# Kernel optimization log

Measured on AMD Instinct MI355X. Metric: run time of the kernel, lower is better.

The kernel has to match this reference:

```python
import jax, jax.numpy as jnp
import numpy as np

B, L, DIM, ET, NH, SD, NC = 32, 200, 36, 128, 64, 9, 2


def setup_inputs() -> dict:
    key = jax.random.key(0)
    ks = jax.random.split(key, 16)
    f = jnp.float32
    vals = jax.random.normal(ks[0], (B, L, DIM), f)
    obs = (jax.random.uniform(ks[1], (B, L, DIM)) < 0.7).astype(f)  # 0/1 observation mask
    x = jnp.concatenate([vals, obs], -1)                            # (B, L, 2*DIM)
    time_steps = jnp.sort(jax.random.uniform(ks[2], (B, L)), axis=1)
    static_info = jax.random.normal(ks[3], (B, SD), f)
    query_param = jnp.linspace(0.0, 1.0, ET, dtype=f)               # nn.Parameter(linspace)

    def lin(k, o, i, s):
        return jax.random.normal(k, (o, i), f) * s

    return dict(
        x=x, time_steps=time_steps, static_info=static_info, query_param=query_param,
        periodic_w=lin(ks[4], ET - 1, 1, 1.0), periodic_b=jnp.zeros((ET - 1,), f),
        timelin_w=lin(ks[5], 1, 1, 1.0), timelin_b=jnp.zeros((1,), f),
        qw=lin(ks[6], ET, ET, ET ** -0.5), qb=jnp.zeros((ET,), f),
        kw=lin(ks[7], ET, ET, ET ** -0.5), kb=jnp.zeros((ET,), f),
        ow=lin(ks[8], DIM, 2 * DIM, (2 * DIM) ** -0.5), ob=jnp.zeros((DIM,), f),
        gru_w_ih=lin(ks[9], 3 * NH, DIM, DIM ** -0.5),
        gru_w_hh=lin(ks[10], 3 * NH, NH, NH ** -0.5),
        gru_b_ih=jnp.zeros((3 * NH,), f), gru_b_hh=jnp.zeros((3 * NH,), f),
        st_w=lin(ks[11], 8, SD, SD ** -0.5), st_b=jnp.zeros((8,), f),
        c1_w=lin(ks[12], NH + 8, NH + 8, (NH + 8) ** -0.5), c1_b=jnp.zeros((NH + 8,), f),
        bn_g=jnp.ones((NH + 8,), f), bn_b=jnp.zeros((NH + 8,), f),
        c2_w=lin(ks[13], NC, NH + 8, (NH + 8) ** -0.5), c2_b=jnp.zeros((NC,), f),
        rand_mask=jax.random.randint(ks[14], (B, L), 0, 2, jnp.int32),
    )


def reference(x, time_steps, static_info, query_param, periodic_w, periodic_b,
              timelin_w, timelin_b, qw, qb, kw, kb, ow, ob,
              gru_w_ih, gru_w_hh, gru_b_ih, gru_b_hh, st_w, st_b,
              c1_w, c1_b, bn_g, bn_b, c2_w, c2_b, rand_mask):
    dim = x.shape[-1] // 2
    irr = x[:, :, dim:]                                   # observation mask channels
    temp = rand_mask.astype(x.dtype)[:, :, None]          # random_masking keep-mask
    m_small = irr * temp
    irr2 = jnp.concatenate([irr, irr], -1)                # (B, L, 2*dim)
    m2 = jnp.concatenate([m_small, m_small], -1)

    def time_emb(tt):
        tt = tt[..., None]
        return jnp.concatenate([tt @ timelin_w.T + timelin_b,
                                jnp.sin(tt @ periodic_w.T + periodic_b)], -1)

    key_e = time_emb(time_steps)                          # (B, L, ET)
    query_e = time_emb(query_param[None, :])[0]           # (ET, ET)
    q = query_e @ qw.T + qb                               # num_heads=1 => dk=ET
    k = key_e @ kw.T + kb
    scores = jnp.einsum('qd,bld->bql', q, k) / jnp.sqrt(jnp.asarray(ET, x.dtype))

    def mta(mask):
        # per-channel masked softmax over keys l: (B, Lq, L, 2*dim)
        s5 = jnp.where(mask[:, None, :, :] == 0, jnp.asarray(-1e9, x.dtype),
                       scores[:, :, :, None])
        p = jax.nn.softmax(s5, axis=2)
        o = jnp.einsum('bqld,bld->bqd', p, x)             # (B, Lq, 2*dim)
        return o @ ow.T + ob                              # (B, Lq, dim)

    out_te = mta(irr2)
    out1_te = mta(m2)

    sx = x[:, :, :dim]
    sx_g = jnp.round(jax.nn.sigmoid(jnp.einsum('bld,ble->bde', sx, sx)))
    sout = jax.nn.sigmoid(jnp.einsum('bqd,bqe->bde', out_te, out_te))

    def step(h, xt):  # torch GRU cell, gate order r,z,n
        gi = xt @ gru_w_ih.T + gru_b_ih
        gh = h @ gru_w_hh.T + gru_b_hh
        ir, iz, inn = jnp.split(gi, 3, -1)
        hr, hz, hn = jnp.split(gh, 3, -1)
        r = jax.nn.sigmoid(ir + hr)
        z = jax.nn.sigmoid(iz + hz)
        n = jnp.tanh(inn + r * hn)
        return (1 - z) * n + z * h, None

    h0 = jnp.zeros((x.shape[0], gru_w_hh.shape[1]), x.dtype)
    h_fin, _ = jax.lax.scan(step, h0, jnp.swapaxes(out_te, 0, 1))

    st = static_info @ st_w.T + st_b
    cls_in = jnp.concatenate([h_fin, st], 1)
    z1 = cls_in @ c1_w.T + c1_b
    mu = z1.mean(0)
    var = z1.var(0)                                       # BatchNorm1d (training stats)
    zn = (z1 - mu) / jnp.sqrt(var + 1e-5) * bn_g + bn_b
    zg = jax.nn.gelu(zn, approximate=False)
    logits = zg @ c2_w.T + c2_b
    return (out_te, out1_te, logits, sx_g, sout, query_param)
```

## Files before the change

### kernel.cpp

```cpp
#include <hip/hip_runtime.h>

#define B_   32
#define L_   200
#define DIM_ 36
#define ET_  128
#define NH_  64
#define SD_  9
#define NC_  2

#define O_TE   0
#define O_T1   147456
#define O_LG   294912
#define O_SXG  294976
#define O_SOUT 336448
#define O_QP   377920

typedef __fp16 half_t;
typedef __attribute__((ext_vector_type(2))) __fp16 half2_t;

__device__ __forceinline__ float sigm(float x) { return 1.f / (1.f + expf(-x)); }
__device__ __forceinline__ float fsigm(float x) {
  return __builtin_amdgcn_rcpf(1.f + __expf(-x));
}
__device__ __forceinline__ float ftanh(float x) {
  return 2.f * __builtin_amdgcn_rcpf(1.f + __expf(-2.f * x)) - 1.f;
}
__device__ __forceinline__ half2_t f2h2(float a, float b) {
  return __builtin_amdgcn_cvt_pkrtz(a, b);
}
__device__ __forceinline__ float dot2acc(half2_t w, half2_t h, float acc) {
#if __has_builtin(__builtin_amdgcn_fdot2)
  return __builtin_amdgcn_fdot2(w, h, acc, false);
#else
  return acc + (float)w.x * (float)h.x + (float)w.y * (float)h.y;
#endif
}

__global__ __launch_bounds__(256) void k_pre2(
    const float* __restrict__ qw, const float* __restrict__ kw,
    const float* __restrict__ qb, const float* __restrict__ qp,
    const float* __restrict__ pw, const float* __restrict__ pb,
    const float* __restrict__ tlw, const float* __restrict__ tlb,
    const float* __restrict__ x, float* __restrict__ qm2,
    float* __restrict__ xmean, float* __restrict__ out) {
  int blk = blockIdx.x, t = threadIdx.x;
  if (blk < 128) {
    __shared__ float eq[128];
    __shared__ float uq[128];
    int q = blk;
    if (t < 128) {
      float tt = qp[q];
      eq[t] = (t == 0) ? tt * tlw[0] + tlb[0]
                       : __sinf(tt * pw[t - 1] + pb[t - 1]);
    }
    __syncthreads();
    if (t < 128) {
      const float4* qw4 = (const float4*)(qw + (size_t)t * 128);
      float a = qb[t];
      #pragma unroll 8
      for (int c = 0; c < 32; c++) {
        float4 w = qw4[c];
        a += eq[4 * c] * w.x + eq[4 * c + 1] * w.y +
             eq[4 * c + 2] * w.z + eq[4 * c + 3] * w.w;
      }
      uq[t] = a;
    }
    __syncthreads();
    if (t < 128) {
      float a = 0.f;
      #pragma unroll 8
      for (int i = 0; i < 128; i++) a += uq[i] * kw[i * 128 + t];
      qm2[q * 128 + t] = a * 0.088388347648318447f;
      if (q == 0) out[O_QP + t] = qp[t];
    }
    return;
  }
  int b = blk - 128;
  __shared__ __align__(16) float sxs[L_][76];
  const float4* xsrc = (const float4*)(x + (size_t)b * L_ * 72);
  for (int idx = t; idx < L_ * 18; idx += 256) {
    int l = idx / 18, c = idx % 18;
    ((float4*)&sxs[l][0])[c] = xsrc[l * 18 + c];
  }
  __syncthreads();
  if (t < 72) {
    float s = 0.f;
    #pragma unroll 8
    for (int l = 0; l < L_; l++) s += sxs[l][t];
    xmean[b * 72 + t] = s * (1.0f / L_);
  }
  for (int idx = t; idx < DIM_ * DIM_; idx += 256) {
    int d = idx / DIM_, e = idx % DIM_;
    float s = 0.f;
    #pragma unroll 8
    for (int l = 0; l < L_; l++) s += sxs[l][d] * sxs[l][e];
    out[O_SXG + (size_t)b * DIM_ * DIM_ + idx] = rintf(sigm(s));
  }
}

__global__ __launch_bounds__(1024, 1) void k_attn(
    const float* __restrict__ qm, const float* __restrict__ ts,
    const float* __restrict__ pw, const float* __restrict__ pb,
    const float* __restrict__ tlw, const float* __restrict__ tlb,
    const float* __restrict__ x, const int* __restrict__ rm,
    const float* __restrict__ xmean, const float* __restrict__ ow,
    const float* __restrict__ ob, const float* __restrict__ wih,
    const float* __restrict__ bih, const float* __restrict__ bhh,
    float* __restrict__ gis, float* __restrict__ out) {
  __shared__ __align__(16) char Abuf[103936];
  __shared__ __align__(16) float qs[16][128];
  __shared__ __align__(16) float sc[16][200];
  __shared__ __align__(16) float owsh[DIM_][72];
  float*   ksA  = (float*)Abuf;
  half2_t* wsh2 = (half2_t*)Abuf;
  float*   wihs = (float*)Abuf;
  float*   ote_t = (float*)(Abuf + 28416);
  float*   sums = (float*)(Abuf + 57600);
  float*   ofr  = (float*)(Abuf + 57600 + 36864);

  int b = blockIdx.x >> 3;
  int q0 = (blockIdx.x & 7) << 4;
  int tid = threadIdx.x;

  const float4* qsrc = (const float4*)(qm + q0 * ET_);
  for (int i = tid; i < 16 * 32; i += 1024) ((float4*)qs)[i] = qsrc[i];
  const float4* owsrc = (const float4*)ow;
  for (int i = tid; i < DIM_ * 18; i += 1024) ((float4*)owsh)[i] = owsrc[i];
  {
    float tl_w = tlw[0], tl_b = tlb[0];
    const float* tsb = ts + b * L_;
    for (int i = tid; i < L_ * 128; i += 1024) {
      int l = i >> 7, j = i & 127;
      float t = tsb[l];
      float e = (j == 0) ? t * tl_w + tl_b : __sinf(t * pw[j - 1] + pb[j - 1]);
      int blkj = (j >> 2) ^ ((l >> 2) & 7);
      ksA[(l << 7) + (blkj << 2) + (j & 3)] = e;
    }
  }
  __syncthreads();

  {
    int w = tid >> 6, lg = tid & 63;
    int qp2 = w >> 1;
    int lh = w & 1;
    float acc[2][2];
    #pragma unroll
    for (int i = 0; i < 2; i++)
      #pragma unroll
      for (int j = 0; j < 2; j++) acc[i][j] = 0.f;
    const float4* ks4 = (const float4*)ksA;
    const float4* qs4 = (const float4*)qs;
    int lbase = 100 * lh + 2 * lg;
    int swz0 = (lbase >> 2) & 7;
    int swz1 = ((lbase + 1) >> 2) & 7;
    #pragma unroll 4
    for (int d4 = 0; d4 < 32; d4++) {
      float4 kv[2];
      {
        int l0c = (lbase < 100 * lh + 100) ? lbase : (100 * lh + 99);
        int l1c = (lbase + 1 < 100 * lh + 100) ? lbase + 1 : (100 * lh + 99);
        kv[0] = ks4[(l0c << 5) + (d4 ^ swz0)];
        kv[1] = ks4[(l1c << 5) + (d4 ^ swz1)];
      }
      #pragma unroll
      for (int i = 0; i < 2; i++) {
        float4 qv = qs4[(2 * qp2 + i) * 32 + d4];
        #pragma unroll
        for (int j = 0; j < 2; j++)
          acc[i][j] += qv.x * kv[j].x + qv.y * kv[j].y +
                       qv.z * kv[j].z + qv.w * kv[j].w;
      }
    }
    if (2 * lg < 100) {
      #pragma unroll
      for (int i = 0; i < 2; i++) {
        float2 v = {acc[i][0], acc[i][1]};
        *((float2*)(&sc[2 * qp2 + i][lbase])) = v;
      }
    }
  }
  __syncthreads();

  {
    int qi = tid >> 6, li = tid & 63;
    float m = -1e30f;
    for (int l = li; l < L_; l += 64) m = fmaxf(m, sc[qi][l]);
    #pragma unroll
    for (int off = 32; off >= 1; off >>= 1) m = fmaxf(m, __shfl_xor(m, off));
    for (int l = li; l < L_; l += 64) sc[qi][l] = __expf(sc[qi][l] - m);
  }

  {
    const float2* xb2 = (const float2*)(x + (size_t)b * L_ * 72);
    const int* rmb = rm + b * L_;
    for (int i = tid; i < L_ * 72; i += 1024) {
      int l = i / 72, c2 = i % 72;
      int seg = c2 / 18, fh = c2 % 18;
      float2 v = xb2[l * 36 + fh];
      float2 o = xb2[l * 36 + 18 + fh];
      float rr = (float)rmb[l];
      float w0, w1;
      if (seg == 0)      { w0 = o.x * v.x;      w1 = o.y * v.y; }
      else if (seg == 1) { w0 = o.x;            w1 = o.y; }
      else if (seg == 2) { w0 = o.x * v.x * rr; w1 = o.y * v.y * rr; }
      else               { w0 = o.x * rr;       w1 = o.y * rr; }
      wsh2[l * 72 + c2] = f2h2(w0, w1);
    }
  }
  __syncthreads();

  {
    int quarter = tid >> 8, tt = tid & 255;
    int qi = tt >> 4, li = tt & 15;
    int l0 = quarter * 50;
    float accA[8], accB[8];
    #pragma unroll
    for (int k = 0; k < 8; k++) { accA[k] = 0.f; accB[k] = 0.f; }
    const float4* wA = (const float4*)wsh2;
    #pragma unroll 2
    for (int l = l0; l < l0 + 50; l++) {
      float ev = sc[qi][l];
      float4 wa = wA[l * 18 + li];
      union { float f; half2_t h; } u0, u1, u2, u3;
      u0.f = wa.x; u1.f = wa.y; u2.f = wa.z; u3.f = wa.w;
      accA[0] += ev * (float)u0.h.x; accA[1] += ev * (float)u0.h.y;
      accA[2] += ev * (float)u1.h.x; accA[3] += ev * (float)u1.h.y;
      accA[4] += ev * (float)u2.h.x; accA[5] += ev * (float)u2.h.y;
      accA[6] += ev * (float)u3.h.x; accA[7] += ev * (float)u3.h.y;
      if (li < 2) {
        float4 wb = wA[l * 18 + 16 + li];
        union { float f; half2_t h; } b0, b1, b2, b3;
        b0.f = wb.x; b1.f = wb.y; b2.f = wb.z; b3.f = wb.w;
        accB[0] += ev * (float)b0.h.x; accB[1] += ev * (float)b0.h.y;
        accB[2] += ev * (float)b1.h.x; accB[3] += ev * (float)b1.h.y;
        accB[4] += ev * (float)b2.h.x; accB[5] += ev * (float)b2.h.y;
        accB[6] += ev * (float)b3.h.x; accB[7] += ev * (float)b3.h.y;
      }
    }
    float* sq = sums + quarter * 2304 + qi * 144;
    float4* sA = (float4*)(sq + 8 * li);
    sA[0] = make_float4(accA[0], accA[1], accA[2], accA[3]);
    sA[1] = make_float4(accA[4], accA[5], accA[6], accA[7]);
    if (li < 2) {
      float4* sB = (float4*)(sq + 128 + 8 * li);
      sB[0] = make_float4(accB[0], accB[1], accB[2], accB[3]);
      sB[1] = make_float4(accB[4], accB[5], accB[6], accB[7]);
    }
  }
  __syncthreads();

  const float* xm = xmean + b * 72;
  for (int idx = tid; idx < 192 * 36; idx += 1024) {
    int r = idx / 36, d = idx % 36;
    wihs[r * 37 + d] = wih[idx];
  }
  for (int idx = tid; idx < 16 * DIM_; idx += 1024) {
    int qq = idx / DIM_, j = idx % DIM_;
    const float* s0 = sums + qq * 144;
    const float* s1 = s0 + 2304;
    const float* s2 = s1 + 2304;
    const float* s3 = s2 + 2304;
    float numA = (s0[j] + s1[j]) + (s2[j] + s3[j]);
    float denA = (s0[36 + j] + s1[36 + j]) + (s2[36 + j] + s3[36 + j]);
    float numB = (s0[72 + j] + s1[72 + j]) + (s2[72 + j] + s3[72 + j]);
    float denB = (s0[108 + j] + s1[108 + j]) + (s2[108 + j] + s3[108 + j]);
    float al, ah, bl, bh;
    if (denA > 0.f) { al = numA / denA; ah = 1.f; }
    else            { al = xm[j];       ah = xm[36 + j]; }
    if (denB > 0.f) { bl = numB / denB; bh = 1.f; }
    else            { bl = xm[j];       bh = xm[36 + j]; }
    float* oq = ofr + qq * 144;
    oq[j] = al;      oq[36 + j] = ah;
    oq[72 + j] = bl; oq[108 + j] = bh;
  }
  __syncthreads();

  for (int idx = tid; idx < 16 * 72; idx += 1024) {
    int qq = idx / 72, t = idx % 72;
    int v = t / DIM_, i2 = t % DIM_;
    const float4* o4 = (const float4*)(ofr + qq * 144 + v * 72);
    const float4* w4 = (const float4*)(owsh[i2]);
    float a = ob[i2];
    #pragma unroll
    for (int d4 = 0; d4 < 18; d4++) {
      float4 ov = o4[d4], wv = w4[d4];
      a += ov.x * wv.x + ov.y * wv.y + ov.z * wv.z + ov.w * wv.w;
    }
    size_t off = ((size_t)b * ET_ + q0 + qq) * DIM_ + i2;
    out[(v == 0 ? O_TE : O_T1) + off] = a;
    if (v == 0) ote_t[qq * 36 + i2] = a;
  }
  __syncthreads();

  for (int idx = tid; idx < 16 * 192; idx += 1024) {
    int qq = idx / 192, tt = idx % 192;
    const float* wr = wihs + tt * 37;
    const float* orow = ote_t + qq * 36;
    float a = bih[tt] + ((tt < 2 * NH_) ? bhh[tt] : 0.f);
    #pragma unroll 6
    for (int d = 0; d < 36; d++) a += orow[d] * wr[d];
    gis[((size_t)b * ET_ + q0 + qq) * 192 + tt] = a;
  }
}

__global__ __launch_bounds__(256, 1) void k_sg(
    const float* __restrict__ out_ro, const float* __restrict__ gis,
    const float* __restrict__ whh, const float* __restrict__ bhh,
    float* __restrict__ hfin, float* __restrict__ out) {
  __shared__ __align__(16) float ote_s[ET_][DIM_];
  __shared__ __align__(16) half2_t hpk[NH_ / 2];
  int blk = blockIdx.x, t = threadIdx.x;

  if (blk < 32) {
    int b = blk;
    const float4* osrc = (const float4*)(out_ro + O_TE + (size_t)b * ET_ * DIM_);
    for (int idx = t; idx < ET_ * 9; idx += 256)
      ((float4*)&ote_s[0][0])[idx] = osrc[idx];
    __syncthreads();
    for (int idx = t; idx < DIM_ * DIM_; idx += 256) {
      int d = idx / DIM_, e = idx % DIM_;
      float s = 0.f;
      #pragma unroll 8
      for (int q = 0; q < ET_; q++) s += ote_s[q][d] * ote_s[q][e];
      out[O_SOUT + (size_t)b * DIM_ * DIM_ + idx] = sigm(s);
    }
    return;
  }

  if (t >= 64) return;
  int b = blk - 32;
  const float* gb = gis + (size_t)b * ET_ * 192;

  half2_t wr[32], wz[32], wn[32];
  {
    const float2* r0 = (const float2*)(whh + (size_t)t * NH_);
    const float2* r1 = (const float2*)(whh + (size_t)(NH_ + t) * NH_);
    const float2* r2 = (const float2*)(whh + (size_t)(2 * NH_ + t) * NH_);
    #pragma unroll
    for (int c = 0; c < 32; c++) {
      float2 a = r0[c], bb = r1[c], cc = r2[c];
      wr[c] = f2h2(a.x, a.y);
      wz[c] = f2h2(bb.x, bb.y);
      wn[c] = f2h2(cc.x, cc.y);
    }
  }
  float bh_n = bhh[2 * NH_ + t];

  float pr[2], pz[2], pn[2];
  pr[0] = gb[t];       pz[0] = gb[64 + t];       pn[0] = gb[128 + t];
  pr[1] = gb[192 + t]; pz[1] = gb[192 + 64 + t]; pn[1] = gb[192 + 128 + t];

  float h = 0.f;
  ((half_t*)hpk)[t] = (half_t)0.f;
  for (int q = 0; q < ET_; q++) {
    int s = q & 1;
    float gi_r = pr[s], gi_z = pz[s], gi_n = pn[s];
    if (q + 2 < ET_) {
      const float* g2 = gb + (q + 2) * 192;
      pr[s] = g2[t]; pz[s] = g2[64 + t]; pn[s] = g2[128 + t];
    }
    float ar = 0.f, az = 0.f, an = 0.f;
    const float4* hp4 = (const float4*)hpk;
    #pragma unroll
    for (int c4 = 0; c4 < 8; c4++) {
      float4 hv = hp4[c4];
      union { float f; half2_t h; } u0, u1, u2, u3;
      u0.f = hv.x; u1.f = hv.y; u2.f = hv.z; u3.f = hv.w;
      int c = c4 * 4;
      ar = dot2acc(wr[c + 0], u0.h, ar);
      az = dot2acc(wz[c + 0], u0.h, az);
      an = dot2acc(wn[c + 0], u0.h, an);
      ar = dot2acc(wr[c + 1], u1.h, ar);
      az = dot2acc(wz[c + 1], u1.h, az);
      an = dot2acc(wn[c + 1], u1.h, an);
      ar = dot2acc(wr[c + 2], u2.h, ar);
      az = dot2acc(wz[c + 2], u2.h, az);
      an = dot2acc(wn[c + 2], u2.h, an);
      ar = dot2acc(wr[c + 3], u3.h, ar);
      az = dot2acc(wz[c + 3], u3.h, az);
      an = dot2acc(wn[c + 3], u3.h, an);
    }
    float r = fsigm(gi_r + ar);
    float z = fsigm(gi_z + az);
    float n = ftanh(gi_n + r * (an + bh_n));
    h = n + z * (h - n);
    ((half_t*)hpk)[t] = (half_t)h;
  }
  hfin[b * NH_ + t] = h;
}

__global__ __launch_bounds__(256) void k_cls(
    const float* __restrict__ hfin, const float* __restrict__ si,
    const float* __restrict__ stw, const float* __restrict__ stb,
    const float* __restrict__ c1w, const float* __restrict__ c1b,
    const float* __restrict__ bng, const float* __restrict__ bnb,
    const float* __restrict__ c2w, const float* __restrict__ c2b,
    float* __restrict__ out) {
  __shared__ float cin[B_][72];
  __shared__ float z1[B_][72];
  __shared__ float zg[B_][72];
  int t = threadIdx.x;
  for (int idx = t; idx < B_ * 8; idx += 256) {
    int b = idx / 8, j = idx % 8;
    float acc = stb[j];
    #pragma unroll
    for (int d = 0; d < SD_; d++) acc += si[b * SD_ + d] * stw[j * SD_ + d];
    cin[b][NH_ + j] = acc;
  }
  for (int idx = t; idx < B_ * NH_; idx += 256)
    cin[idx / NH_][idx % NH_] = hfin[idx];
  __syncthreads();
  for (int idx = t; idx < B_ * 72; idx += 256) {
    int b = idx / 72, j = idx % 72;
    float acc = c1b[j];
    #pragma unroll 8
    for (int d = 0; d < 72; d++) acc += cin[b][d] * c1w[j * 72 + d];
    z1[b][j] = acc;
  }
  __syncthreads();
  if (t < 72) {
    float mu = 0.f;
    for (int b = 0; b < B_; b++) mu += z1[b][t];
    mu *= (1.f / B_);
    float vv = 0.f;
    for (int b = 0; b < B_; b++) { float d = z1[b][t] - mu; vv += d * d; }
    vv *= (1.f / B_);
    float inv = 1.f / sqrtf(vv + 1e-5f);
    float g = bng[t], bb = bnb[t];
    for (int b = 0; b < B_; b++) {
      float zn = (z1[b][t] - mu) * inv * g + bb;
      zg[b][t] = 0.5f * zn * (1.f + erff(zn * 0.70710678118654752f));
    }
  }
  __syncthreads();
  for (int idx = t; idx < B_ * NC_; idx += 256) {
    int b = idx / NC_, c = idx % NC_;
    float acc = c2b[c];
    #pragma unroll 8
    for (int d = 0; d < 72; d++) acc += zg[b][d] * c2w[c * 72 + d];
    out[O_LG + idx] = acc;
  }
}

extern "C" void kernel_launch(void* const* d_in, const int* in_sizes, int n_in,
                              void* d_out, int out_size, void* d_ws,
                              size_t ws_size, hipStream_t stream) {
  const float* x    = (const float*)d_in[0];
  const float* ts   = (const float*)d_in[1];
  const float* si   = (const float*)d_in[2];
  const float* qp   = (const float*)d_in[3];
  const float* pw   = (const float*)d_in[4];
  const float* pb   = (const float*)d_in[5];
  const float* tlw  = (const float*)d_in[6];
  const float* tlb  = (const float*)d_in[7];
  const float* qw   = (const float*)d_in[8];
  const float* qb   = (const float*)d_in[9];
  const float* kw   = (const float*)d_in[10];
  const float* ow   = (const float*)d_in[12];
  const float* ob   = (const float*)d_in[13];
  const float* wih  = (const float*)d_in[14];
  const float* whh  = (const float*)d_in[15];
  const float* bih  = (const float*)d_in[16];
  const float* bhh  = (const float*)d_in[17];
  const float* stw  = (const float*)d_in[18];
  const float* stb  = (const float*)d_in[19];
  const float* c1w  = (const float*)d_in[20];
  const float* c1b  = (const float*)d_in[21];
  const float* bng  = (const float*)d_in[22];
  const float* bnb  = (const float*)d_in[23];
  const float* c2w  = (const float*)d_in[24];
  const float* c2b  = (const float*)d_in[25];
  const int*   rm   = (const int*)d_in[26];

  float* out = (float*)d_out;

  float* W = (float*)d_ws;
  float* ws_qm2   = W;
  float* ws_xmean = W + 16384;
  float* ws_hfin  = W + 18688;
  float* ws_gis   = W + 20736;

  hipLaunchKernelGGL(k_pre2, dim3(160), dim3(256), 0, stream,
                     qw, kw, qb, qp, pw, pb, tlw, tlb, x, ws_qm2, ws_xmean,
                     out);
  hipLaunchKernelGGL(k_attn, dim3(B_ * 8), dim3(1024), 0, stream,
                     ws_qm2, ts, pw, pb, tlw, tlb, x, rm, ws_xmean, ow, ob,
                     wih, bih, bhh, ws_gis, out);
  hipLaunchKernelGGL(k_sg, dim3(64), dim3(256), 0, stream,
                     out, ws_gis, whh, bhh, ws_hfin, out);
  hipLaunchKernelGGL(k_cls, dim3(1), dim3(256), 0, stream,
                     ws_hfin, si, stw, stb, c1w, c1b, bng, bnb, c2w, c2b,
                     out);
}
```

Measured before the change: 263.4 us.

## Move GRU input projection from attention kernel into the GRU kernel via shared memory

The GRU input-gate projection (out_te @ W_ih^T + biases) is no longer computed at the end of the attention kernel and written to a global workspace. Instead, each GRU block loads its batch's out_te into shared memory and computes all 128x192 gate inputs into a shared array before the recurrence. This removes a global round trip, an extra sync and the W_ih staging from k_attn, and turns the per-step gate loads into shared reads. The cost is that the projection work moves onto only 32 GRU blocks, using 192 threads each, on the serial critical path.

```diff
diff --git a/kernel.cpp b/kernel.cpp
--- a/kernel.cpp
+++ b/kernel.cpp
@@ -104,17 +104,13 @@
     const float* __restrict__ tlw, const float* __restrict__ tlb,
     const float* __restrict__ x, const int* __restrict__ rm,
     const float* __restrict__ xmean, const float* __restrict__ ow,
-    const float* __restrict__ ob, const float* __restrict__ wih,
-    const float* __restrict__ bih, const float* __restrict__ bhh,
-    float* __restrict__ gis, float* __restrict__ out) {
+    const float* __restrict__ ob, float* __restrict__ out) {
   __shared__ __align__(16) char Abuf[103936];
   __shared__ __align__(16) float qs[16][128];
   __shared__ __align__(16) float sc[16][200];
   __shared__ __align__(16) float owsh[DIM_][72];
   float*   ksA  = (float*)Abuf;
   half2_t* wsh2 = (half2_t*)Abuf;
-  float*   wihs = (float*)Abuf;
-  float*   ote_t = (float*)(Abuf + 28416);
   float*   sums = (float*)(Abuf + 57600);
   float*   ofr  = (float*)(Abuf + 57600 + 36864);
 
@@ -250,10 +246,6 @@
   __syncthreads();
 
   const float* xm = xmean + b * 72;
-  for (int idx = tid; idx < 192 * 36; idx += 1024) {
-    int r = idx / 36, d = idx % 36;
-    wihs[r * 37 + d] = wih[idx];
-  }
   for (int idx = tid; idx < 16 * DIM_; idx += 1024) {
     int qq = idx / DIM_, j = idx % DIM_;
     const float* s0 = sums + qq * 144;
@@ -288,26 +280,16 @@
     }
     size_t off = ((size_t)b * ET_ + q0 + qq) * DIM_ + i2;
     out[(v == 0 ? O_TE : O_T1) + off] = a;
-    if (v == 0) ote_t[qq * 36 + i2] = a;
-  }
-  __syncthreads();
-
-  for (int idx = tid; idx < 16 * 192; idx += 1024) {
-    int qq = idx / 192, tt = idx % 192;
-    const float* wr = wihs + tt * 37;
-    const float* orow = ote_t + qq * 36;
-    float a = bih[tt] + ((tt < 2 * NH_) ? bhh[tt] : 0.f);
-    #pragma unroll 6
-    for (int d = 0; d < 36; d++) a += orow[d] * wr[d];
-    gis[((size_t)b * ET_ + q0 + qq) * 192 + tt] = a;
   }
 }
 
 __global__ __launch_bounds__(256, 1) void k_sg(
-    const float* __restrict__ out_ro, const float* __restrict__ gis,
-    const float* __restrict__ whh, const float* __restrict__ bhh,
-    float* __restrict__ hfin, float* __restrict__ out) {
+    const float* __restrict__ out_ro, const float* __restrict__ wih,
+    const float* __restrict__ bih, const float* __restrict__ whh,
+    const float* __restrict__ bhh, float* __restrict__ hfin,
+    float* __restrict__ out) {
   __shared__ __align__(16) float ote_s[ET_][DIM_];
+  __shared__ float gis[ET_][3 * NH_];
   __shared__ __align__(16) half2_t hpk[NH_ / 2];
   int blk = blockIdx.x, t = threadIdx.x;
 
@@ -327,9 +309,33 @@
     return;
   }
 
+  int b = blk - 32;
+  const float* ote = out_ro + O_TE;
+  const float4* osrc = (const float4*)(ote + (size_t)b * ET_ * DIM_);
+  for (int idx = t; idx < ET_ * DIM_ / 4; idx += 256)
+    ((float4*)&ote_s[0][0])[idx] = osrc[idx];
+  __syncthreads();
+
+  if (t < 3 * NH_) {
+    float wv[DIM_];
+    const float* wrow = wih + (size_t)t * DIM_;
+    #pragma unroll
+    for (int d = 0; d < DIM_; d++) wv[d] = wrow[d];
+    float bi = bih[t] + ((t < 2 * NH_) ? bhh[t] : 0.f);
+    for (int q = 0; q < ET_; q++) {
+      const float4* xr = (const float4*)ote_s[q];
+      float a = bi;
+      #pragma unroll
+      for (int c = 0; c < 9; c++) {
+        float4 xv = xr[c];
+        a += xv.x * wv[4 * c] + xv.y * wv[4 * c + 1] +
+             xv.z * wv[4 * c + 2] + xv.w * wv[4 * c + 3];
+      }
+      gis[q][t] = a;
+    }
+  }
+  __syncthreads();
   if (t >= 64) return;
-  int b = blk - 32;
-  const float* gb = gis + (size_t)b * ET_ * 192;
 
   half2_t wr[32], wz[32], wn[32];
   {
@@ -346,19 +352,12 @@
   }
   float bh_n = bhh[2 * NH_ + t];
 
-  float pr[2], pz[2], pn[2];
-  pr[0] = gb[t];       pz[0] = gb[64 + t];       pn[0] = gb[128 + t];
-  pr[1] = gb[192 + t]; pz[1] = gb[192 + 64 + t]; pn[1] = gb[192 + 128 + t];
-
   float h = 0.f;
   ((half_t*)hpk)[t] = (half_t)0.f;
   for (int q = 0; q < ET_; q++) {
-    int s = q & 1;
-    float gi_r = pr[s], gi_z = pz[s], gi_n = pn[s];
-    if (q + 2 < ET_) {
-      const float* g2 = gb + (q + 2) * 192;
-      pr[s] = g2[t]; pz[s] = g2[64 + t]; pn[s] = g2[128 + t];
-    }
+    float gi_r = gis[q][t];
+    float gi_z = gis[q][NH_ + t];
+    float gi_n = gis[q][2 * NH_ + t];
     float ar = 0.f, az = 0.f, an = 0.f;
     const float4* hp4 = (const float4*)hpk;
     #pragma unroll
@@ -478,16 +477,15 @@
   float* ws_qm2   = W;
   float* ws_xmean = W + 16384;
   float* ws_hfin  = W + 18688;
-  float* ws_gis   = W + 20736;
 
   hipLaunchKernelGGL(k_pre2, dim3(160), dim3(256), 0, stream,
                      qw, kw, qb, qp, pw, pb, tlw, tlb, x, ws_qm2, ws_xmean,
                      out);
   hipLaunchKernelGGL(k_attn, dim3(B_ * 8), dim3(1024), 0, stream,
                      ws_qm2, ts, pw, pb, tlw, tlb, x, rm, ws_xmean, ow, ob,
-                     wih, bih, bhh, ws_gis, out);
+                     out);
   hipLaunchKernelGGL(k_sg, dim3(64), dim3(256), 0, stream,
-                     out, ws_gis, whh, bhh, ws_hfin, out);
+                     out, wih, bih, whh, bhh, ws_hfin, out);
   hipLaunchKernelGGL(k_cls, dim3(1), dim3(256), 0, stream,
                      ws_hfin, si, stw, stb, c1w, c1b, bng, bnb, c2w, c2b,
                      out);
```

New measurement: 246.7 us. 1.07x faster.
